# Optimization experiments

Measured on AMD Instinct MI355X. Metric: run time of the kernel, lower is better.

The kernel has to match this reference:

```python
import jax, jax.numpy as jnp
import numpy as np
from math import sqrt

V, D, H, HD, L, F, P, NL = 32000, 768, 12, 64, 12, 3072, 2048, 2
B, S = 8, 1024
EPS = 1e-5


def setup_inputs() -> dict:
    key = jax.random.key(0)
    ks = jax.random.split(key, 12)
    n = lambda k, sh: (jax.random.normal(k, sh, jnp.float32) * 0.02)
    return {
        'tokens': jax.random.randint(ks[0], (B, S), 0, V, dtype=jnp.int32),
        'tok_emb': n(ks[1], (V, D)),
        'pos_emb': n(ks[2], (P, D)),
        'emb_ln_s': jnp.ones((D,), jnp.float32), 'emb_ln_b': jnp.zeros((D,), jnp.float32),
        'Wq': n(ks[3], (L, H, D, HD)), 'bq': jnp.zeros((L, H, HD), jnp.float32),
        'Wk': n(ks[4], (L, H, D, HD)), 'bk': jnp.zeros((L, H, HD), jnp.float32),
        'Wv': n(ks[5], (L, H, D, HD)), 'bv': jnp.zeros((L, H, HD), jnp.float32),
        'Wo': n(ks[6], (L, D, D)), 'bo': jnp.zeros((L, D), jnp.float32),
        'ln1_s': jnp.ones((L, D), jnp.float32), 'ln1_b': jnp.zeros((L, D), jnp.float32),
        'ln2_s': jnp.ones((L, D), jnp.float32), 'ln2_b': jnp.zeros((L, D), jnp.float32),
        'W1': n(ks[7], (L, D, F)), 'b1': jnp.zeros((L, F), jnp.float32),
        'W2': n(ks[8], (L, F, D)), 'b2': jnp.zeros((L, D), jnp.float32),
        'Wc': n(ks[9], (D, NL)), 'bc': jnp.zeros((NL,), jnp.float32),
    }


def _ln(x, s, b):
    m = jnp.mean(x, -1, keepdims=True)
    v = jnp.mean((x - m) ** 2, -1, keepdims=True)
    return (x - m) * jax.lax.rsqrt(v + EPS) * s + b


def reference(tokens, tok_emb, pos_emb, emb_ln_s, emb_ln_b,
              Wq, bq, Wk, bk, Wv, bv, Wo, bo,
              ln1_s, ln1_b, ln2_s, ln2_b, W1, b1, W2, b2, Wc, bc):
    b, s = tokens.shape
    # embeddings (dropout is eval-mode identity)
    x = tok_emb[tokens] + pos_emb[:s][None, :, :]          # [b, s, D]
    x = _ln(x, emb_ln_s, emb_ln_b)
    scale = 1.0 / sqrt(HD)
    for l in range(L):
        xn = _ln(x, ln1_s[l], ln1_b[l])
        q = jnp.einsum('bsd,hdk->bhsk', xn, Wq[l]) + bq[l][:, None, :]
        k = jnp.einsum('bsd,hdk->bhsk', xn, Wk[l]) + bk[l][:, None, :]
        v = jnp.einsum('bsd,hdk->bhsk', xn, Wv[l]) + bv[l][:, None, :]
        scores = jnp.einsum('bhsk,bhtk->bhst', q, k) * scale   # [b,H,s,s]
        w = jax.nn.softmax(scores, axis=-1)
        o = jnp.einsum('bhst,bhtk->bhsk', w, v)                # [b,H,s,HD]
        o = o.transpose(0, 2, 1, 3).reshape(b, s, D)           # concat heads
        x = x + o @ Wo[l] + bo[l]
        xn = _ln(x, ln2_s[l], ln2_b[l])
        h = jax.nn.gelu(xn @ W1[l] + b1[l], approximate=False)
        x = x + h @ W2[l] + b2[l]
    # CLS token -> classifier (dropout identity)
    return x[:, 0, :] @ Wc + bc                                # [b, NL]
```

## Files before the change

### kernel.cpp

```cpp
#include <hip/hip_runtime.h>
#include <hip/hip_bf16.h>
#include <math.h>

#define B_   8
#define S_   1024
#define D_   768
#define H_   12
#define HD_  64
#define L_   12
#define F_   3072
#define NTOK 8192

typedef __bf16 bf16x8 __attribute__((ext_vector_type(8)));
typedef float  f32x4  __attribute__((ext_vector_type(4)));
typedef unsigned short u16;

static __device__ __forceinline__ unsigned short f2bf_bits(float f) {
    __hip_bfloat16 h = __float2bfloat16(f);
    return __builtin_bit_cast(unsigned short, h);
}
static __device__ __forceinline__ float bf2f(unsigned short u) {
    unsigned int t = ((unsigned int)u) << 16;
    return __builtin_bit_cast(float, t);
}
static __device__ __forceinline__ void gload16(const void* g, void* l) {
    __builtin_amdgcn_global_load_lds(
        (__attribute__((address_space(1))) void*)g,
        (__attribute__((address_space(3))) void*)l, 16, 0, 0);
}

__global__ __launch_bounds__(256)
void prep_layer_kernel(const float* __restrict__ Wq, const float* __restrict__ Wk,
                       const float* __restrict__ Wv, const float* __restrict__ Wo,
                       const float* __restrict__ W1, const float* __restrict__ W2,
                       int l, __hip_bfloat16* __restrict__ wbuf)
{
    const int id = blockIdx.x;
    const float* src; __hip_bfloat16* dst;
    int R, C, r0, c0;
    if (id < 432) {
        int dtile = id % 12, t = id / 12;
        int which = t / 12, h = t % 12;
        src = (which == 0 ? Wq : which == 1 ? Wk : Wv) + (size_t)(l*12 + h) * 768 * 64;
        dst = wbuf + (size_t)(which*768 + h*64) * 768;
        R = 768; C = 64; r0 = dtile * 64; c0 = 0;
    } else if (id < 576) {
        int t = id - 432;
        src = Wo + (size_t)l * 768 * 768;
        dst = wbuf + 1769472;
        R = 768; C = 768; r0 = (t / 12) * 64; c0 = (t % 12) * 64;
    } else if (id < 1152) {
        int t = id - 576;
        src = W1 + (size_t)l * 768 * 3072;
        dst = wbuf + 2359296;
        R = 768; C = 3072; r0 = (t % 12) * 64; c0 = (t / 12) * 64;
    } else {
        int t = id - 1152;
        src = W2 + (size_t)l * 3072 * 768;
        dst = wbuf + 4718592;
        R = 3072; C = 768; r0 = (t / 12) * 64; c0 = (t % 12) * 64;
    }
    __shared__ u16 T[64][68];
    const int t = threadIdx.x;
    const int row = t >> 2, part = t & 3;
#pragma unroll
    for (int j = 0; j < 4; ++j) {
        const int c4 = (part + j*4) * 4;
        float4 v = *(const float4*)(src + (size_t)(r0 + row) * C + c0 + c4);
        T[c4+0][row] = f2bf_bits(v.x);
        T[c4+1][row] = f2bf_bits(v.y);
        T[c4+2][row] = f2bf_bits(v.z);
        T[c4+3][row] = f2bf_bits(v.w);
    }
    __syncthreads();
    const int c = t >> 2;
    u16* drow = (u16*)dst + (size_t)(c0 + c) * R + r0;
#pragma unroll
    for (int j = 0; j < 4; ++j) {
        const int r4 = (part + j*4) * 4;
        ushort4 pk = *(const ushort4*)&T[c][r4];
        *(ushort4*)(drow + r4) = pk;
    }
}

__global__ __launch_bounds__(256)
void prep_bqkv_kernel(const float* __restrict__ bq, const float* __restrict__ bk,
                      const float* __restrict__ bv, float* __restrict__ bqkv)
{
    int i = blockIdx.x * 256 + threadIdx.x;
    int l = i / 2304, c = i % 2304;
    int which = c / 768, hk = c % 768;
    const float* src = which == 0 ? bq : which == 1 ? bk : bv;
    bqkv[i] = src[l*768 + hk];
}

__global__ __launch_bounds__(256)
void embed_ln_kernel(const int* __restrict__ tokens, const float* __restrict__ tok_emb,
                     const float* __restrict__ pos_emb, const float* __restrict__ gam,
                     const float* __restrict__ bet, float* __restrict__ x)
{
    const int row  = blockIdx.x*4 + (threadIdx.x >> 6);
    const int lane = threadIdx.x & 63;
    const int s    = row & (S_-1);
    const int tok  = tokens[row];
    const float* te = tok_emb + (size_t)tok * D_;
    const float* pe = pos_emb + (size_t)s   * D_;
    float v[12]; float s1 = 0.f, s2 = 0.f;
#pragma unroll
    for (int c = 0; c < 3; ++c) {
        const int base = c*256 + lane*4;
        float4 a = *(const float4*)(te + base);
        float4 p = *(const float4*)(pe + base);
        float t0 = a.x+p.x, t1 = a.y+p.y, t2 = a.z+p.z, t3 = a.w+p.w;
        v[c*4+0]=t0; v[c*4+1]=t1; v[c*4+2]=t2; v[c*4+3]=t3;
        s1 += t0+t1+t2+t3;
        s2 += t0*t0 + t1*t1 + t2*t2 + t3*t3;
    }
#pragma unroll
    for (int off = 32; off > 0; off >>= 1) { s1 += __shfl_xor(s1, off); s2 += __shfl_xor(s2, off); }
    const float mean = s1 * (1.f/768.f);
    const float rstd = rsqrtf(s2*(1.f/768.f) - mean*mean + 1e-5f);
    float* xr = x + (size_t)row * D_;
#pragma unroll
    for (int c = 0; c < 3; ++c) {
        const int base = c*256 + lane*4;
        float4 g = *(const float4*)(gam + base);
        float4 bb = *(const float4*)(bet + base);
        float4 o;
        o.x = (v[c*4+0]-mean)*rstd*g.x + bb.x;
        o.y = (v[c*4+1]-mean)*rstd*g.y + bb.y;
        o.z = (v[c*4+2]-mean)*rstd*g.z + bb.z;
        o.w = (v[c*4+3]-mean)*rstd*g.w + bb.w;
        *(float4*)(xr + base) = o;
    }
}

__global__ __launch_bounds__(256)
void ln_kernel(const float* __restrict__ xin, const float* __restrict__ gam,
               const float* __restrict__ bet, __hip_bfloat16* __restrict__ out)
{
    const int row  = blockIdx.x*4 + (threadIdx.x >> 6);
    const int lane = threadIdx.x & 63;
    const float* xr = xin + (size_t)row * D_;
    float v[12]; float s1 = 0.f, s2 = 0.f;
#pragma unroll
    for (int c = 0; c < 3; ++c) {
        float4 t = *(const float4*)(xr + c*256 + lane*4);
        v[c*4+0]=t.x; v[c*4+1]=t.y; v[c*4+2]=t.z; v[c*4+3]=t.w;
        s1 += t.x+t.y+t.z+t.w;
        s2 += t.x*t.x + t.y*t.y + t.z*t.z + t.w*t.w;
    }
#pragma unroll
    for (int off = 32; off > 0; off >>= 1) { s1 += __shfl_xor(s1, off); s2 += __shfl_xor(s2, off); }
    const float mean = s1 * (1.f/768.f);
    const float rstd = rsqrtf(s2*(1.f/768.f) - mean*mean + 1e-5f);
    unsigned short* op = (unsigned short*)out + (size_t)row * D_;
#pragma unroll
    for (int c = 0; c < 3; ++c) {
        const int base = c*256 + lane*4;
        float4 g = *(const float4*)(gam + base);
        float4 bb = *(const float4*)(bet + base);
        ushort4 pk;
        pk.x = f2bf_bits((v[c*4+0]-mean)*rstd*g.x + bb.x);
        pk.y = f2bf_bits((v[c*4+1]-mean)*rstd*g.y + bb.y);
        pk.z = f2bf_bits((v[c*4+2]-mean)*rstd*g.z + bb.z);
        pk.w = f2bf_bits((v[c*4+3]-mean)*rstd*g.w + bb.w);
        *(ushort4*)(op + base) = pk;
    }
}

template<int EPI>
__global__ __launch_bounds__(256)
void gemm_kernel(const __hip_bfloat16* __restrict__ A,
                 const __hip_bfloat16* __restrict__ Bt,
                 const float* __restrict__ bias,
                 __hip_bfloat16* __restrict__ outb,
                 __hip_bfloat16* __restrict__ outv,
                 int N, int K, int nTiles)
{
    __shared__ __align__(16) char smem[32768];
    __hip_bfloat16* As = (__hip_bfloat16*)smem;
    __hip_bfloat16* Bs = (__hip_bfloat16*)(smem + 16384);

    const int tid  = threadIdx.x;
    const int lane = tid & 63;
    const int wid  = tid >> 6;

    const int nwg   = gridDim.x;
    const int chunk = nwg >> 3;
    const int bid   = blockIdx.x;
    const int swz   = (bid & 7) * chunk + (bid >> 3);
    const int m0 = (swz / nTiles) * 128;
    const int n0 = (swz % nTiles) * 128;

    const int srow = wid*32 + (lane >> 3);
    const int scol = ((lane & 7) ^ (srow & 7)) * 8;
    const __hip_bfloat16* aSrc = A  + (size_t)(m0 + srow) * K + scol;
    const __hip_bfloat16* bSrc = Bt + (size_t)(n0 + srow) * K + scol;
    char* aDst = (char*)As + wid*4096 + lane*16;
    char* bDst = (char*)Bs + wid*4096 + lane*16;

    f32x4 acc[4][4] = {};
    const int wm = wid >> 1, wn = wid & 1;
    const int cl = lane & 15, hi = lane >> 4;

    for (int kt = 0; kt < K; kt += 64) {
        __syncthreads();
#pragma unroll
        for (int i = 0; i < 4; ++i)
            gload16(aSrc + kt + (size_t)i*8*K, aDst + i*1024);
#pragma unroll
        for (int i = 0; i < 4; ++i)
            gload16(bSrc + kt + (size_t)i*8*K, bDst + i*1024);
        __syncthreads();

#pragma unroll
        for (int kk = 0; kk < 2; ++kk) {
            bf16x8 af[4], bfr[4];
#pragma unroll
            for (int m = 0; m < 4; ++m) {
                int row  = wm*64 + m*16 + cl;
                int slot = ((kk<<2) + hi) ^ (row & 7);
                af[m] = *(const bf16x8*)((const char*)As + row*128 + slot*16);
            }
#pragma unroll
            for (int n = 0; n < 4; ++n) {
                int row  = wn*64 + n*16 + cl;
                int slot = ((kk<<2) + hi) ^ (row & 7);
                bfr[n] = *(const bf16x8*)((const char*)Bs + row*128 + slot*16);
            }
#pragma unroll
            for (int m = 0; m < 4; ++m)
#pragma unroll
                for (int n = 0; n < 4; ++n)
                    acc[m][n] = __builtin_amdgcn_mfma_f32_16x16x32_bf16(af[m], bfr[n], acc[m][n], 0, 0, 0);
        }
    }

    const bool vpath = (EPI == 0) && (n0 >= 1536);

    if (!vpath) {
        __syncthreads();
#pragma unroll
        for (int n = 0; n < 4; ++n) {
            const int col2 = wn*64 + n*16 + cl;
            const float bv = bias[n0 + col2];
#pragma unroll
            for (int m = 0; m < 4; ++m) {
#pragma unroll
                for (int i = 0; i < 4; ++i) {
                    const int row = wm*64 + m*16 + hi*4 + i;
                    float v = acc[m][n][i] + bv;
                    if constexpr (EPI == 1) {
                        const float y = 0.7978845608f * (v + 0.044715f*v*v*v);
                        const float e = __expf(-2.0f * fabsf(y));
                        const float th = (1.0f - e) / (1.0f + e);
                        v = 0.5f * v * (1.0f + copysignf(th, y));
                    }
                    *(u16*)(smem + row*256 + ((((col2 >> 3) ^ (row & 15))) << 4)
                                 + ((col2 & 7) << 1)) = f2bf_bits(v);
                }
            }
        }
        __syncthreads();
        const int strideN = (EPI == 0) ? 1536 : N;
        const int r  = tid >> 1;
        const int cb = tid & 1;
        char* dst = (char*)outb + ((size_t)(m0 + r) * strideN + n0) * 2;
#pragma unroll
        for (int j = 0; j < 8; ++j) {
            const int ch = cb + j*2;
            float4 vv = *(const float4*)(smem + r*256 + ((ch ^ (r & 15)) << 4));
            *(float4*)(dst + ch*16) = vv;
        }
    } else {
        __syncthreads();
#pragma unroll
        for (int n = 0; n < 4; ++n) {
            const int col = n0 + wn*64 + n*16 + cl;
            const float bv = bias[col];
            const int hdl = wn*64 + n*16 + cl;
#pragma unroll
            for (int m = 0; m < 4; ++m) {
                const int sl = wm*64 + m*16 + hi*4;
                ushort4 pk;
                pk.x = f2bf_bits(acc[m][n][0] + bv);
                pk.y = f2bf_bits(acc[m][n][1] + bv);
                pk.z = f2bf_bits(acc[m][n][2] + bv);
                pk.w = f2bf_bits(acc[m][n][3] + bv);
                *(ushort4*)(smem + hdl*256 + ((((sl >> 3) ^ (hdl & 15))) << 4) + (sl & 7)*2) = pk;
            }
        }
        __syncthreads();
        const int hdl2 = tid >> 1;
        const int sh   = (tid & 1) * 64;
        const int hdg  = (n0 - 1536) + hdl2;
        const int bb   = m0 >> 10;
        u16* dst = (u16*)outv + ((size_t)(bb*768) + hdg)*1024 + (m0 & 1023) + sh;
#pragma unroll
        for (int j = 0; j < 8; ++j) {
            const int slot = ((sh >> 3) + j) ^ (hdl2 & 15);
            *(float4*)((char*)dst + j*16) = *(const float4*)(smem + hdl2*256 + (slot << 4));
        }
    }
}

__global__ __launch_bounds__(256)
void gemm64_res_kernel(const __hip_bfloat16* __restrict__ A,
                       const __hip_bfloat16* __restrict__ Bt,
                       const float* __restrict__ bias,
                       float* __restrict__ outf,
                       int N, int K, int nTiles)
{
    __shared__ __align__(16) char smem[32768];
    __hip_bfloat16* As = (__hip_bfloat16*)smem;
    __hip_bfloat16* Bs = (__hip_bfloat16*)(smem + 8192);

    const int tid  = threadIdx.x;
    const int lane = tid & 63;
    const int wid  = tid >> 6;

    const int nwg   = gridDim.x;
    const int chunk = nwg >> 3;
    const int bid   = blockIdx.x;
    const int swz   = (bid & 7) * chunk + (bid >> 3);
    const int m0 = (swz / nTiles) * 64;
    const int n0 = (swz % nTiles) * 128;

    const int lrow = lane >> 3;
    const int scol = ((lane & 7) ^ lrow) * 8;
    const __hip_bfloat16* aSrc = A  + (size_t)(m0 + wid*16 + lrow) * K + scol;
    const __hip_bfloat16* bSrc = Bt + (size_t)(n0 + wid*32 + lrow) * K + scol;
    char* aDst = (char*)As + wid*2048 + lane*16;
    char* bDst = (char*)Bs + wid*4096 + lane*16;

    f32x4 acc[2][4] = {};
    const int wm = wid >> 1, wn = wid & 1;
    const int cl = lane & 15, hi = lane >> 4;

    for (int kt = 0; kt < K; kt += 64) {
        __syncthreads();
#pragma unroll
        for (int i = 0; i < 2; ++i)
            gload16(aSrc + kt + (size_t)i*8*K, aDst + i*1024);
#pragma unroll
        for (int i = 0; i < 4; ++i)
            gload16(bSrc + kt + (size_t)i*8*K, bDst + i*1024);
        __syncthreads();

#pragma unroll
        for (int kk = 0; kk < 2; ++kk) {
            bf16x8 af[2], bfr[4];
#pragma unroll
            for (int m = 0; m < 2; ++m) {
                int row  = wm*32 + m*16 + cl;
                int slot = ((kk<<2) + hi) ^ (row & 7);
                af[m] = *(const bf16x8*)((const char*)As + row*128 + slot*16);
            }
#pragma unroll
            for (int n = 0; n < 4; ++n) {
                int row  = wn*64 + n*16 + cl;
                int slot = ((kk<<2) + hi) ^ (row & 7);
                bfr[n] = *(const bf16x8*)((const char*)Bs + row*128 + slot*16);
            }
#pragma unroll
            for (int m = 0; m < 2; ++m)
#pragma unroll
                for (int n = 0; n < 4; ++n)
                    acc[m][n] = __builtin_amdgcn_mfma_f32_16x16x32_bf16(af[m], bfr[n], acc[m][n], 0, 0, 0);
        }
    }

    __syncthreads();
#pragma unroll
    for (int n = 0; n < 4; ++n) {
        const int col = wn*64 + n*16 + cl;
        const float bv = bias[n0 + col];
#pragma unroll
        for (int m = 0; m < 2; ++m) {
#pragma unroll
            for (int i = 0; i < 4; ++i) {
                const int row = wm*32 + m*16 + hi*4 + i;
                *(float*)(smem + row*512 + ((((col >> 2) ^ (row & 31))) << 4)
                               + ((col & 3) << 2)) = acc[m][n][i] + bv;
            }
        }
    }
    __syncthreads();
    const int r = tid >> 2;
    const int part = tid & 3;
    float* drow = outf + (size_t)(m0 + r) * N + n0;
#pragma unroll
    for (int j = 0; j < 8; ++j) {
        const int ch = part + j*4;
        f32x4 vv = *(const f32x4*)(smem + r*512 + ((ch ^ (r & 31)) << 4));
        float* dp = drow + ch*4;
        f32x4 g = *(const f32x4*)dp;
        g += vv;
        *(f32x4*)dp = g;
    }
}

__global__ __launch_bounds__(512)
void attn_kernel(const __hip_bfloat16* __restrict__ qkb, const __hip_bfloat16* __restrict__ vtb,
                 __hip_bfloat16* __restrict__ attno)
{
    __shared__ __align__(16) char Ks[2][8192];
    __shared__ __align__(16) char Vs[2][8192];
    __shared__ __align__(16) char Ps[16384];

    const u16* qk = (const u16*)qkb;
    const u16* vt = (const u16*)vtb;
    const int nwg = gridDim.x, bid = blockIdx.x, chunk = nwg >> 3;
    const int swz = (bid & 7) * chunk + (bid >> 3);
    const int bh = swz >> 3, qb = swz & 7;
    const int b = bh / H_, h = bh % H_;
    const int tid = threadIdx.x;
    const int lane = tid & 63, wid = tid >> 6;
    const int cl = lane & 15, hi = lane >> 4;
    const size_t browq = (size_t)(b*S_ + qb*128);

    bf16x8 qf[2];
    {
        const u16* qp = qk + (browq + wid*16 + cl)*1536 + h*64;
        qf[0] = *(const bf16x8*)(qp + hi*8);
        qf[1] = *(const bf16x8*)(qp + 32 + hi*8);
    }

    const int lrow = lane >> 3;
    const int scol = ((lane & 7) ^ lrow) * 8;
    const u16* kbase = qk + ((size_t)b*S_ + wid*8 + lrow)*1536 + 768 + h*64 + scol;
    const u16* vbase = vt + (((size_t)(b*H_ + h))*64 + wid*8 + lrow)*1024 + scol;
    const int ldst = wid*1024 + lane*16;

    f32x4 acc_o[4] = {};
    float m_run = -1e30f;
    float l_part[4] = {0.f, 0.f, 0.f, 0.f};
    char* pbase = Ps + wid*2048;

    {
        gload16(kbase, Ks[0] + ldst);
        gload16(vbase, Vs[0] + ldst);
    }

    for (int t = 0; t < 16; ++t) {
        __syncthreads();
        if (t < 15) {
            const int nb = (t+1) & 1;
            gload16(kbase + (size_t)(t+1)*64*1536, Ks[nb] + ldst);
            gload16(vbase + (t+1)*64,              Vs[nb] + ldst);
        }
        const char* ks = Ks[t & 1];
        const char* vs = Vs[t & 1];

        f32x4 sc[4] = {};
#pragma unroll
        for (int kk = 0; kk < 2; ++kk) {
            bf16x8 kf[4];
#pragma unroll
            for (int n = 0; n < 4; ++n) {
                const int row = n*16 + cl;
                kf[n] = *(const bf16x8*)(ks + row*128 + (((kk*4 + hi) ^ (cl & 7)) << 4));
            }
#pragma unroll
            for (int n = 0; n < 4; ++n)
                sc[n] = __builtin_amdgcn_mfma_f32_16x16x32_bf16(qf[kk], kf[n], sc[n], 0, 0, 0);
        }

#pragma unroll
        for (int n = 0; n < 4; ++n)
#pragma unroll
            for (int i = 0; i < 4; ++i)
                sc[n][i] *= 0.125f;

        float gmax = sc[0][0];
#pragma unroll
        for (int n = 0; n < 4; ++n)
#pragma unroll
            for (int i = 0; i < 4; ++i)
                gmax = fmaxf(gmax, sc[n][i]);
        gmax = fmaxf(gmax, __shfl_xor(gmax, 1));
        gmax = fmaxf(gmax, __shfl_xor(gmax, 2));
        gmax = fmaxf(gmax, __shfl_xor(gmax, 4));
        gmax = fmaxf(gmax, __shfl_xor(gmax, 8));
        if (gmax > m_run + 4.0f) {
            const float corr = __expf(m_run - gmax);
            m_run = gmax;
#pragma unroll
            for (int i = 0; i < 4; ++i) l_part[i] *= corr;
#pragma unroll
            for (int nd = 0; nd < 4; ++nd)
#pragma unroll
                for (int i = 0; i < 4; ++i)
                    acc_o[nd][i] *= corr;
        }

#pragma unroll
        for (int n = 0; n < 4; ++n) {
#pragma unroll
            for (int i = 0; i < 4; ++i) {
                const float e = __expf(sc[n][i] - m_run);
                l_part[i] += e;
                const int q = hi*4 + i;
                const int slot = (n*2 + (cl >> 3)) ^ (q & 7);
                *(u16*)(pbase + q*128 + slot*16 + (cl & 7)*2) = f2bf_bits(e);
            }
        }

        asm volatile("s_waitcnt lgkmcnt(0)" ::: "memory");
        __builtin_amdgcn_sched_barrier(0);

#pragma unroll
        for (int kk = 0; kk < 2; ++kk) {
            const bf16x8 pf = *(const bf16x8*)(pbase + cl*128 + (((kk*4 + hi) ^ (cl & 7)) << 4));
            bf16x8 vf[4];
#pragma unroll
            for (int nd = 0; nd < 4; ++nd) {
                const int d = nd*16 + cl;
                vf[nd] = *(const bf16x8*)(vs + d*128 + (((kk*4 + hi) ^ (d & 7)) << 4));
            }
#pragma unroll
            for (int nd = 0; nd < 4; ++nd)
                acc_o[nd] = __builtin_amdgcn_mfma_f32_16x16x32_bf16(pf, vf[nd], acc_o[nd], 0, 0, 0);
        }
    }

    u16* op = (u16*)attno;
#pragma unroll
    for (int i = 0; i < 4; ++i) {
        float l = l_part[i];
        l += __shfl_xor(l, 1);
        l += __shfl_xor(l, 2);
        l += __shfl_xor(l, 4);
        l += __shfl_xor(l, 8);
        const float inv = 1.f / l;
        const size_t row = browq + wid*16 + hi*4 + i;
#pragma unroll
        for (int nd = 0; nd < 4; ++nd)
            op[row*768 + h*64 + nd*16 + cl] = f2bf_bits(acc_o[nd][i] * inv);
    }
}

__global__ __launch_bounds__(256)
void cls_kernel(const float* __restrict__ x, const float* __restrict__ Wc,
                const float* __restrict__ bc, float* __restrict__ out)
{
    const int b = blockIdx.x;
    const float* xr = x + (size_t)b * S_ * D_;
    float a0 = 0.f, a1 = 0.f;
    for (int d = threadIdx.x; d < 768; d += 256) {
        float xv = xr[d];
        a0 += xv * Wc[d*2+0];
        a1 += xv * Wc[d*2+1];
    }
#pragma unroll
    for (int off = 32; off > 0; off >>= 1) { a0 += __shfl_xor(a0, off); a1 += __shfl_xor(a1, off); }
    __shared__ float r0[4], r1[4];
    const int w = threadIdx.x >> 6;
    if ((threadIdx.x & 63) == 0) { r0[w] = a0; r1[w] = a1; }
    __syncthreads();
    if (threadIdx.x == 0) {
        out[b*2+0] = r0[0]+r0[1]+r0[2]+r0[3] + bc[0];
        out[b*2+1] = r1[0]+r1[1]+r1[2]+r1[3] + bc[1];
    }
}

extern "C" void kernel_launch(void* const* d_in, const int* in_sizes, int n_in,
                              void* d_out, int out_size, void* d_ws, size_t ws_size,
                              hipStream_t stream)
{
    const int*   tokens  = (const int*)  d_in[0];
    const float* tok_emb = (const float*)d_in[1];
    const float* pos_emb = (const float*)d_in[2];
    const float* e_s     = (const float*)d_in[3];
    const float* e_b     = (const float*)d_in[4];
    const float* Wq      = (const float*)d_in[5];
    const float* bq      = (const float*)d_in[6];
    const float* Wk      = (const float*)d_in[7];
    const float* bk      = (const float*)d_in[8];
    const float* Wv      = (const float*)d_in[9];
    const float* bv      = (const float*)d_in[10];
    const float* Wo      = (const float*)d_in[11];
    const float* bo      = (const float*)d_in[12];
    const float* l1s     = (const float*)d_in[13];
    const float* l1b     = (const float*)d_in[14];
    const float* l2s     = (const float*)d_in[15];
    const float* l2b     = (const float*)d_in[16];
    const float* W1      = (const float*)d_in[17];
    const float* b1      = (const float*)d_in[18];
    const float* W2      = (const float*)d_in[19];
    const float* b2      = (const float*)d_in[20];
    const float* Wc      = (const float*)d_in[21];
    const float* bc      = (const float*)d_in[22];
    (void)in_sizes; (void)n_in; (void)out_size;

    if (ws_size < 102346752) return;

    char* ws = (char*)d_ws;
    __hip_bfloat16* wbuf = (__hip_bfloat16*)(ws + 0);
    float*          bqkv = (float*)(ws + 14155776);
    float*          x    = (float*)(ws + 14266368);
    __hip_bfloat16* xn   = (__hip_bfloat16*)(ws + 39432192);
    __hip_bfloat16* qk   = (__hip_bfloat16*)(ws + 52015104);
    __hip_bfloat16* vT   = (__hip_bfloat16*)(ws + 77180928);
    __hip_bfloat16* att  = (__hip_bfloat16*)(ws + 89763840);
    __hip_bfloat16* hbuf = qk;

    __hip_bfloat16* wqkv_t = wbuf;
    __hip_bfloat16* wo_t   = wbuf + 1769472;
    __hip_bfloat16* w1_t   = wbuf + 2359296;
    __hip_bfloat16* w2_t   = wbuf + 4718592;

    prep_bqkv_kernel<<<108, 256, 0, stream>>>(bq, bk, bv, bqkv);
    embed_ln_kernel<<<2048, 256, 0, stream>>>(tokens, tok_emb, pos_emb, e_s, e_b, x);

    for (int l = 0; l < L_; ++l) {
        prep_layer_kernel<<<1728, 256, 0, stream>>>(Wq, Wk, Wv, Wo, W1, W2, l, wbuf);
        ln_kernel<<<2048, 256, 0, stream>>>(x, l1s + l*768, l1b + l*768, xn);
        gemm_kernel<0><<<1152, 256, 0, stream>>>(xn, wqkv_t, bqkv + l*2304, qk, vT, 2304, 768, 18);
        attn_kernel<<<768, 512, 0, stream>>>(qk, vT, att);
        gemm64_res_kernel<<<768, 256, 0, stream>>>(att, wo_t, bo + l*768, x, 768, 768, 6);
        ln_kernel<<<2048, 256, 0, stream>>>(x, l2s + l*768, l2b + l*768, xn);
        gemm_kernel<1><<<1536, 256, 0, stream>>>(xn, w1_t, b1 + l*3072, hbuf, nullptr, 3072, 768, 24);
        gemm64_res_kernel<<<768, 256, 0, stream>>>(hbuf, w2_t, b2 + l*768, x, 768, 3072, 6);
    }
    cls_kernel<<<8, 256, 0, stream>>>(x, Wc, bc, (float*)d_out);
}
```

Before: 3.232 ms.

## Double-buffer GEMM shared tiles and unify on 64x128 tiles across all projections

```diff
diff --git a/kernel.cpp b/kernel.cpp
--- a/kernel.cpp
+++ b/kernel.cpp
@@ -176,11 +176,14 @@
                  const float* __restrict__ bias,
                  __hip_bfloat16* __restrict__ outb,
                  __hip_bfloat16* __restrict__ outv,
+                 float* __restrict__ outf,
                  int N, int K, int nTiles)
 {
-    __shared__ __align__(16) char smem[32768];
-    __hip_bfloat16* As = (__hip_bfloat16*)smem;
-    __hip_bfloat16* Bs = (__hip_bfloat16*)(smem + 16384);
+    __shared__ __align__(16) char smem[49152];
+    char* const As0 = smem;
+    char* const As1 = smem + 8192;
+    char* const Bs0 = smem + 16384;
+    char* const Bs1 = smem + 32768;
 
     const int tid  = threadIdx.x;
     const int lane = tid & 63;
@@ -190,66 +193,108 @@
     const int chunk = nwg >> 3;
     const int bid   = blockIdx.x;
     const int swz   = (bid & 7) * chunk + (bid >> 3);
-    const int m0 = (swz / nTiles) * 128;
+    const int m0 = (swz / nTiles) * 64;
     const int n0 = (swz % nTiles) * 128;
 
-    const int srow = wid*32 + (lane >> 3);
-    const int scol = ((lane & 7) ^ (srow & 7)) * 8;
-    const __hip_bfloat16* aSrc = A  + (size_t)(m0 + srow) * K + scol;
-    const __hip_bfloat16* bSrc = Bt + (size_t)(n0 + srow) * K + scol;
-    char* aDst = (char*)As + wid*4096 + lane*16;
-    char* bDst = (char*)Bs + wid*4096 + lane*16;
-
-    f32x4 acc[4][4] = {};
+    const int lrow = lane >> 3;
+    const int scol = ((lane & 7) ^ lrow) * 8;
+    const __hip_bfloat16* aSrc = A  + (size_t)(m0 + wid*16 + lrow) * K + scol;
+    const __hip_bfloat16* bSrc = Bt + (size_t)(n0 + wid*32 + lrow) * K + scol;
+    const int aOff = wid*2048 + lane*16;
+    const int bOff = wid*4096 + lane*16;
+
+    f32x4 acc[2][4] = {};
     const int wm = wid >> 1, wn = wid & 1;
     const int cl = lane & 15, hi = lane >> 4;
 
-    for (int kt = 0; kt < K; kt += 64) {
+#pragma unroll
+    for (int i = 0; i < 2; ++i)
+        gload16(aSrc + (size_t)i*8*K, As0 + aOff + i*1024);
+#pragma unroll
+    for (int i = 0; i < 4; ++i)
+        gload16(bSrc + (size_t)i*8*K, Bs0 + bOff + i*1024);
+
+    int buf = 0;
+    for (int kt = 0; kt < K; kt += 64, buf ^= 1) {
         __syncthreads();
-#pragma unroll
-        for (int i = 0; i < 4; ++i)
-            gload16(aSrc + kt + (size_t)i*8*K, aDst + i*1024);
-#pragma unroll
-        for (int i = 0; i < 4; ++i)
-            gload16(bSrc + kt + (size_t)i*8*K, bDst + i*1024);
-        __syncthreads();
+        if (kt + 64 < K) {
+            char* an = buf ? As0 : As1;
+            char* bn = buf ? Bs0 : Bs1;
+#pragma unroll
+            for (int i = 0; i < 2; ++i)
+                gload16(aSrc + kt + 64 + (size_t)i*8*K, an + aOff + i*1024);
+#pragma unroll
+            for (int i = 0; i < 4; ++i)
+                gload16(bSrc + kt + 64 + (size_t)i*8*K, bn + bOff + i*1024);
+        }
+        const char* ac = buf ? As1 : As0;
+        const char* bc = buf ? Bs1 : Bs0;
 
 #pragma unroll
         for (int kk = 0; kk < 2; ++kk) {
-            bf16x8 af[4], bfr[4];
-#pragma unroll
-            for (int m = 0; m < 4; ++m) {
-                int row  = wm*64 + m*16 + cl;
+            bf16x8 af[2], bfr[4];
+#pragma unroll
+            for (int m = 0; m < 2; ++m) {
+                int row  = wm*32 + m*16 + cl;
                 int slot = ((kk<<2) + hi) ^ (row & 7);
-                af[m] = *(const bf16x8*)((const char*)As + row*128 + slot*16);
+                af[m] = *(const bf16x8*)(ac + row*128 + slot*16);
             }
 #pragma unroll
             for (int n = 0; n < 4; ++n) {
                 int row  = wn*64 + n*16 + cl;
                 int slot = ((kk<<2) + hi) ^ (row & 7);
-                bfr[n] = *(const bf16x8*)((const char*)Bs + row*128 + slot*16);
-            }
-#pragma unroll
-            for (int m = 0; m < 4; ++m)
+                bfr[n] = *(const bf16x8*)(bc + row*128 + slot*16);
+            }
+#pragma unroll
+            for (int m = 0; m < 2; ++m)
 #pragma unroll
                 for (int n = 0; n < 4; ++n)
                     acc[m][n] = __builtin_amdgcn_mfma_f32_16x16x32_bf16(af[m], bfr[n], acc[m][n], 0, 0, 0);
         }
     }
 
+    __syncthreads();
+
     const bool vpath = (EPI == 0) && (n0 >= 1536);
 
-    if (!vpath) {
+    if constexpr (EPI == 2) {
+#pragma unroll
+        for (int n = 0; n < 4; ++n) {
+            const int col = wn*64 + n*16 + cl;
+            const float bv = bias[n0 + col];
+#pragma unroll
+            for (int m = 0; m < 2; ++m) {
+#pragma unroll
+                for (int i = 0; i < 4; ++i) {
+                    const int row = wm*32 + m*16 + hi*4 + i;
+                    *(float*)(smem + row*512 + ((((col >> 2) ^ (row & 31))) << 4)
+                                   + ((col & 3) << 2)) = acc[m][n][i] + bv;
+                }
+            }
+        }
         __syncthreads();
+        const int r = tid >> 2;
+        const int part = tid & 3;
+        float* drow = outf + (size_t)(m0 + r) * N + n0;
+#pragma unroll
+        for (int j = 0; j < 8; ++j) {
+            const int ch = part + j*4;
+            f32x4 vv = *(const f32x4*)(smem + r*512 + ((ch ^ (r & 31)) << 4));
+            float* dp = drow + ch*4;
+            f32x4 g = *(const f32x4*)dp;
+            g += vv;
+            *(f32x4*)dp = g;
+        }
+    } else if (!vpath) {
 #pragma unroll
         for (int n = 0; n < 4; ++n) {
             const int col2 = wn*64 + n*16 + cl;
             const float bv = bias[n0 + col2];
 #pragma unroll
-            for (int m = 0; m < 4; ++m) {
+            for (int m = 0; m < 2; ++m) {
 #pragma unroll
                 for (int i = 0; i < 4; ++i) {
-                    const int row = wm*64 + m*16 + hi*4 + i;
+                    const int row = wm*32 + m*16 + hi*4 + i;
                     float v = acc[m][n][i] + bv;
                     if constexpr (EPI == 1) {
                         const float y = 0.7978845608f * (v + 0.044715f*v*v*v);
@@ -264,140 +309,42 @@
         }
         __syncthreads();
         const int strideN = (EPI == 0) ? 1536 : N;
-        const int r  = tid >> 1;
-        const int cb = tid & 1;
-        char* dst = (char*)outb + ((size_t)(m0 + r) * strideN + n0) * 2;
-#pragma unroll
-        for (int j = 0; j < 8; ++j) {
-            const int ch = cb + j*2;
+        const int r  = tid >> 2;
+        const int part = tid & 3;
+        u16* dst = (u16*)outb + (size_t)(m0 + r) * strideN + n0;
+#pragma unroll
+        for (int j = 0; j < 4; ++j) {
+            const int ch = part + j*4;
             float4 vv = *(const float4*)(smem + r*256 + ((ch ^ (r & 15)) << 4));
-            *(float4*)(dst + ch*16) = vv;
+            *(float4*)((char*)dst + ch*16) = vv;
         }
     } else {
-        __syncthreads();
 #pragma unroll
         for (int n = 0; n < 4; ++n) {
-            const int col = n0 + wn*64 + n*16 + cl;
-            const float bv = bias[col];
             const int hdl = wn*64 + n*16 + cl;
-#pragma unroll
-            for (int m = 0; m < 4; ++m) {
-                const int sl = wm*64 + m*16 + hi*4;
+            const float bv = bias[n0 + hdl];
+#pragma unroll
+            for (int m = 0; m < 2; ++m) {
+                const int sl = wm*32 + m*16 + hi*4;
                 ushort4 pk;
                 pk.x = f2bf_bits(acc[m][n][0] + bv);
                 pk.y = f2bf_bits(acc[m][n][1] + bv);
                 pk.z = f2bf_bits(acc[m][n][2] + bv);
                 pk.w = f2bf_bits(acc[m][n][3] + bv);
-                *(ushort4*)(smem + hdl*256 + ((((sl >> 3) ^ (hdl & 15))) << 4) + (sl & 7)*2) = pk;
+                *(ushort4*)(smem + hdl*128 + ((((sl >> 3) ^ (hdl & 7))) << 4) + (sl & 7)*2) = pk;
             }
         }
         __syncthreads();
         const int hdl2 = tid >> 1;
-        const int sh   = (tid & 1) * 64;
+        const int sh   = (tid & 1) * 32;
         const int hdg  = (n0 - 1536) + hdl2;
         const int bb   = m0 >> 10;
         u16* dst = (u16*)outv + ((size_t)(bb*768) + hdg)*1024 + (m0 & 1023) + sh;
 #pragma unroll
-        for (int j = 0; j < 8; ++j) {
-            const int slot = ((sh >> 3) + j) ^ (hdl2 & 15);
-            *(float4*)((char*)dst + j*16) = *(const float4*)(smem + hdl2*256 + (slot << 4));
-        }
-    }
-}
-
-__global__ __launch_bounds__(256)
-void gemm64_res_kernel(const __hip_bfloat16* __restrict__ A,
-                       const __hip_bfloat16* __restrict__ Bt,
-                       const float* __restrict__ bias,
-                       float* __restrict__ outf,
-                       int N, int K, int nTiles)
-{
-    __shared__ __align__(16) char smem[32768];
-    __hip_bfloat16* As = (__hip_bfloat16*)smem;
-    __hip_bfloat16* Bs = (__hip_bfloat16*)(smem + 8192);
-
-    const int tid  = threadIdx.x;
-    const int lane = tid & 63;
-    const int wid  = tid >> 6;
-
-    const int nwg   = gridDim.x;
-    const int chunk = nwg >> 3;
-    const int bid   = blockIdx.x;
-    const int swz   = (bid & 7) * chunk + (bid >> 3);
-    const int m0 = (swz / nTiles) * 64;
-    const int n0 = (swz % nTiles) * 128;
-
-    const int lrow = lane >> 3;
-    const int scol = ((lane & 7) ^ lrow) * 8;
-    const __hip_bfloat16* aSrc = A  + (size_t)(m0 + wid*16 + lrow) * K + scol;
-    const __hip_bfloat16* bSrc = Bt + (size_t)(n0 + wid*32 + lrow) * K + scol;
-    char* aDst = (char*)As + wid*2048 + lane*16;
-    char* bDst = (char*)Bs + wid*4096 + lane*16;
-
-    f32x4 acc[2][4] = {};
-    const int wm = wid >> 1, wn = wid & 1;
-    const int cl = lane & 15, hi = lane >> 4;
-
-    for (int kt = 0; kt < K; kt += 64) {
-        __syncthreads();
-#pragma unroll
-        for (int i = 0; i < 2; ++i)
-            gload16(aSrc + kt + (size_t)i*8*K, aDst + i*1024);
-#pragma unroll
-        for (int i = 0; i < 4; ++i)
-            gload16(bSrc + kt + (size_t)i*8*K, bDst + i*1024);
-        __syncthreads();
-
-#pragma unroll
-        for (int kk = 0; kk < 2; ++kk) {
-            bf16x8 af[2], bfr[4];
-#pragma unroll
-            for (int m = 0; m < 2; ++m) {
-                int row  = wm*32 + m*16 + cl;
-                int slot = ((kk<<2) + hi) ^ (row & 7);
-                af[m] = *(const bf16x8*)((const char*)As + row*128 + slot*16);
-            }
-#pragma unroll
-            for (int n = 0; n < 4; ++n) {
-                int row  = wn*64 + n*16 + cl;
-                int slot = ((kk<<2) + hi) ^ (row & 7);
-                bfr[n] = *(const bf16x8*)((const char*)Bs + row*128 + slot*16);
-            }
-#pragma unroll
-            for (int m = 0; m < 2; ++m)
-#pragma unroll
-                for (int n = 0; n < 4; ++n)
-                    acc[m][n] = __builtin_amdgcn_mfma_f32_16x16x32_bf16(af[m], bfr[n], acc[m][n], 0, 0, 0);
-        }
-    }
-
-    __syncthreads();
-#pragma unroll
-    for (int n = 0; n < 4; ++n) {
-        const int col = wn*64 + n*16 + cl;
-        const float bv = bias[n0 + col];
-#pragma unroll
-        for (int m = 0; m < 2; ++m) {
-#pragma unroll
-            for (int i = 0; i < 4; ++i) {
-                const int row = wm*32 + m*16 + hi*4 + i;
-                *(float*)(smem + row*512 + ((((col >> 2) ^ (row & 31))) << 4)
-                               + ((col & 3) << 2)) = acc[m][n][i] + bv;
-            }
-        }
-    }
-    __syncthreads();
-    const int r = tid >> 2;
-    const int part = tid & 3;
-    float* drow = outf + (size_t)(m0 + r) * N + n0;
-#pragma unroll
-    for (int j = 0; j < 8; ++j) {
-        const int ch = part + j*4;
-        f32x4 vv = *(const f32x4*)(smem + r*512 + ((ch ^ (r & 31)) << 4));
-        float* dp = drow + ch*4;
-        f32x4 g = *(const f32x4*)dp;
-        g += vv;
-        *(f32x4*)dp = g;
+        for (int j = 0; j < 4; ++j) {
+            const int slot = ((sh >> 3) + j) ^ (hdl2 & 7);
+            *(float4*)((char*)dst + j*16) = *(const float4*)(smem + hdl2*128 + (slot << 4));
+        }
     }
 }
 
@@ -617,12 +564,12 @@
     for (int l = 0; l < L_; ++l) {
         prep_layer_kernel<<<1728, 256, 0, stream>>>(Wq, Wk, Wv, Wo, W1, W2, l, wbuf);
         ln_kernel<<<2048, 256, 0, stream>>>(x, l1s + l*768, l1b + l*768, xn);
-        gemm_kernel<0><<<1152, 256, 0, stream>>>(xn, wqkv_t, bqkv + l*2304, qk, vT, 2304, 768, 18);
+        gemm_kernel<0><<<2304, 256, 0, stream>>>(xn, wqkv_t, bqkv + l*2304, qk, vT, nullptr, 2304, 768, 18);
         attn_kernel<<<768, 512, 0, stream>>>(qk, vT, att);
-        gemm64_res_kernel<<<768, 256, 0, stream>>>(att, wo_t, bo + l*768, x, 768, 768, 6);
+        gemm_kernel<2><<<768, 256, 0, stream>>>(att, wo_t, bo + l*768, nullptr, nullptr, x, 768, 768, 6);
         ln_kernel<<<2048, 256, 0, stream>>>(x, l2s + l*768, l2b + l*768, xn);
-        gemm_kernel<1><<<1536, 256, 0, stream>>>(xn, w1_t, b1 + l*3072, hbuf, nullptr, 3072, 768, 24);
-        gemm64_res_kernel<<<768, 256, 0, stream>>>(hbuf, w2_t, b2 + l*768, x, 768, 3072, 6);
+        gemm_kernel<1><<<3072, 256, 0, stream>>>(xn, w1_t, b1 + l*3072, hbuf, nullptr, nullptr, 3072, 768, 24);
+        gemm_kernel<2><<<768, 256, 0, stream>>>(hbuf, w2_t, b2 + l*768, nullptr, nullptr, x, 768, 3072, 6);
     }
     cls_kernel<<<8, 256, 0, stream>>>(x, Wc, bc, (float*)d_out);
 }
```

Result: faster. 3.005 ms (-7.0%).

## Double-buffer LDS tiles in GEMM kernels to overlap global loads with MFMA

Applied to the files above, without the earlier changes.

```diff
diff --git a/kernel.cpp b/kernel.cpp
--- a/kernel.cpp
+++ b/kernel.cpp
@@ -171,16 +171,18 @@
 
 template<int EPI>
 __global__ __launch_bounds__(256)
-void gemm_kernel(const __hip_bfloat16* __restrict__ A,
-                 const __hip_bfloat16* __restrict__ Bt,
-                 const float* __restrict__ bias,
-                 __hip_bfloat16* __restrict__ outb,
-                 __hip_bfloat16* __restrict__ outv,
-                 int N, int K, int nTiles)
+void gemm128_kernel(const __hip_bfloat16* __restrict__ A,
+                    const __hip_bfloat16* __restrict__ Bt,
+                    const float* __restrict__ bias,
+                    __hip_bfloat16* __restrict__ outb,
+                    __hip_bfloat16* __restrict__ outv,
+                    int N, int K, int nTiles)
 {
     __shared__ __align__(16) char smem[32768];
-    __hip_bfloat16* As = (__hip_bfloat16*)smem;
-    __hip_bfloat16* Bs = (__hip_bfloat16*)(smem + 16384);
+    char* const As0 = smem;
+    char* const As1 = smem + 8192;
+    char* const Bs0 = smem + 16384;
+    char* const Bs1 = smem + 24576;
 
     const int tid  = threadIdx.x;
     const int lane = tid & 63;
@@ -193,54 +195,66 @@
     const int m0 = (swz / nTiles) * 128;
     const int n0 = (swz % nTiles) * 128;
 
-    const int srow = wid*32 + (lane >> 3);
-    const int scol = ((lane & 7) ^ (srow & 7)) * 8;
-    const __hip_bfloat16* aSrc = A  + (size_t)(m0 + srow) * K + scol;
-    const __hip_bfloat16* bSrc = Bt + (size_t)(n0 + srow) * K + scol;
-    char* aDst = (char*)As + wid*4096 + lane*16;
-    char* bDst = (char*)Bs + wid*4096 + lane*16;
+    const int l4 = lane >> 2;
+    const int sswz = ((lane & 3) ^ ((l4 >> 1) & 3)) * 8;
+    const __hip_bfloat16* aSrc = A  + (size_t)(m0 + wid*32 + l4) * K + sswz;
+    const __hip_bfloat16* bSrc = Bt + (size_t)(n0 + wid*32 + l4) * K + sswz;
+    const int sOff = wid*2048 + lane*16;
 
     f32x4 acc[4][4] = {};
     const int wm = wid >> 1, wn = wid & 1;
     const int cl = lane & 15, hi = lane >> 4;
 
-    for (int kt = 0; kt < K; kt += 64) {
+    int aoff[4], boff[4];
+#pragma unroll
+    for (int m = 0; m < 4; ++m) {
+        const int row = wm*64 + m*16 + cl;
+        aoff[m] = row*64 + ((hi ^ ((row >> 1) & 3)) << 4);
+    }
+#pragma unroll
+    for (int n = 0; n < 4; ++n) {
+        const int row = wn*64 + n*16 + cl;
+        boff[n] = row*64 + ((hi ^ ((row >> 1) & 3)) << 4);
+    }
+
+#pragma unroll
+    for (int i = 0; i < 2; ++i) {
+        gload16(aSrc + (size_t)i*16*K, As0 + sOff + i*1024);
+        gload16(bSrc + (size_t)i*16*K, Bs0 + sOff + i*1024);
+    }
+
+    int buf = 0;
+    for (int kt = 0; kt < K; kt += 32, buf ^= 1) {
         __syncthreads();
-#pragma unroll
-        for (int i = 0; i < 4; ++i)
-            gload16(aSrc + kt + (size_t)i*8*K, aDst + i*1024);
-#pragma unroll
-        for (int i = 0; i < 4; ++i)
-            gload16(bSrc + kt + (size_t)i*8*K, bDst + i*1024);
-        __syncthreads();
-
-#pragma unroll
-        for (int kk = 0; kk < 2; ++kk) {
-            bf16x8 af[4], bfr[4];
-#pragma unroll
-            for (int m = 0; m < 4; ++m) {
-                int row  = wm*64 + m*16 + cl;
-                int slot = ((kk<<2) + hi) ^ (row & 7);
-                af[m] = *(const bf16x8*)((const char*)As + row*128 + slot*16);
-            }
-#pragma unroll
-            for (int n = 0; n < 4; ++n) {
-                int row  = wn*64 + n*16 + cl;
-                int slot = ((kk<<2) + hi) ^ (row & 7);
-                bfr[n] = *(const bf16x8*)((const char*)Bs + row*128 + slot*16);
-            }
-#pragma unroll
-            for (int m = 0; m < 4; ++m)
-#pragma unroll
-                for (int n = 0; n < 4; ++n)
-                    acc[m][n] = __builtin_amdgcn_mfma_f32_16x16x32_bf16(af[m], bfr[n], acc[m][n], 0, 0, 0);
-        }
-    }
+        if (kt + 32 < K) {
+            char* an = buf ? As0 : As1;
+            char* bn = buf ? Bs0 : Bs1;
+#pragma unroll
+            for (int i = 0; i < 2; ++i) {
+                gload16(aSrc + kt + 32 + (size_t)i*16*K, an + sOff + i*1024);
+                gload16(bSrc + kt + 32 + (size_t)i*16*K, bn + sOff + i*1024);
+            }
+        }
+        const char* ac = buf ? As1 : As0;
+        const char* bc = buf ? Bs1 : Bs0;
+
+        bf16x8 af[4], bfr[4];
+#pragma unroll
+        for (int m = 0; m < 4; ++m) af[m]  = *(const bf16x8*)(ac + aoff[m]);
+#pragma unroll
+        for (int n = 0; n < 4; ++n) bfr[n] = *(const bf16x8*)(bc + boff[n]);
+#pragma unroll
+        for (int m = 0; m < 4; ++m)
+#pragma unroll
+            for (int n = 0; n < 4; ++n)
+                acc[m][n] = __builtin_amdgcn_mfma_f32_16x16x32_bf16(af[m], bfr[n], acc[m][n], 0, 0, 0);
+    }
+
+    __syncthreads();
 
     const bool vpath = (EPI == 0) && (n0 >= 1536);
 
     if (!vpath) {
-        __syncthreads();
 #pragma unroll
         for (int n = 0; n < 4; ++n) {
             const int col2 = wn*64 + n*16 + cl;
@@ -274,12 +288,10 @@
             *(float4*)(dst + ch*16) = vv;
         }
     } else {
-        __syncthreads();
 #pragma unroll
         for (int n = 0; n < 4; ++n) {
-            const int col = n0 + wn*64 + n*16 + cl;
-            const float bv = bias[col];
             const int hdl = wn*64 + n*16 + cl;
+            const float bv = bias[n0 + hdl];
 #pragma unroll
             for (int m = 0; m < 4; ++m) {
                 const int sl = wm*64 + m*16 + hi*4;
@@ -306,15 +318,17 @@
 }
 
 __global__ __launch_bounds__(256)
-void gemm64_res_kernel(const __hip_bfloat16* __restrict__ A,
-                       const __hip_bfloat16* __restrict__ Bt,
-                       const float* __restrict__ bias,
-                       float* __restrict__ outf,
-                       int N, int K, int nTiles)
-{
-    __shared__ __align__(16) char smem[32768];
-    __hip_bfloat16* As = (__hip_bfloat16*)smem;
-    __hip_bfloat16* Bs = (__hip_bfloat16*)(smem + 8192);
+void gemm_res_kernel(const __hip_bfloat16* __restrict__ A,
+                     const __hip_bfloat16* __restrict__ Bt,
+                     const float* __restrict__ bias,
+                     float* __restrict__ outf,
+                     int N, int K, int nTiles)
+{
+    __shared__ __align__(16) char smem[49152];
+    char* const As0 = smem;
+    char* const As1 = smem + 8192;
+    char* const Bs0 = smem + 16384;
+    char* const Bs1 = smem + 32768;
 
     const int tid  = threadIdx.x;
     const int lane = tid & 63;
@@ -331,22 +345,35 @@
     const int scol = ((lane & 7) ^ lrow) * 8;
     const __hip_bfloat16* aSrc = A  + (size_t)(m0 + wid*16 + lrow) * K + scol;
     const __hip_bfloat16* bSrc = Bt + (size_t)(n0 + wid*32 + lrow) * K + scol;
-    char* aDst = (char*)As + wid*2048 + lane*16;
-    char* bDst = (char*)Bs + wid*4096 + lane*16;
+    const int aOff = wid*2048 + lane*16;
+    const int bOff = wid*4096 + lane*16;
 
     f32x4 acc[2][4] = {};
     const int wm = wid >> 1, wn = wid & 1;
     const int cl = lane & 15, hi = lane >> 4;
 
-    for (int kt = 0; kt < K; kt += 64) {
+#pragma unroll
+    for (int i = 0; i < 2; ++i)
+        gload16(aSrc + (size_t)i*8*K, As0 + aOff + i*1024);
+#pragma unroll
+    for (int i = 0; i < 4; ++i)
+        gload16(bSrc + (size_t)i*8*K, Bs0 + bOff + i*1024);
+
+    int buf = 0;
+    for (int kt = 0; kt < K; kt += 64, buf ^= 1) {
         __syncthreads();
-#pragma unroll
-        for (int i = 0; i < 2; ++i)
-            gload16(aSrc + kt + (size_t)i*8*K, aDst + i*1024);
-#pragma unroll
-        for (int i = 0; i < 4; ++i)
-            gload16(bSrc + kt + (size_t)i*8*K, bDst + i*1024);
-        __syncthreads();
+        if (kt + 64 < K) {
+            char* an = buf ? As0 : As1;
+            char* bn = buf ? Bs0 : Bs1;
+#pragma unroll
+            for (int i = 0; i < 2; ++i)
+                gload16(aSrc + kt + 64 + (size_t)i*8*K, an + aOff + i*1024);
+#pragma unroll
+            for (int i = 0; i < 4; ++i)
+                gload16(bSrc + kt + 64 + (size_t)i*8*K, bn + bOff + i*1024);
+        }
+        const char* ac = buf ? As1 : As0;
+        const char* bc = buf ? Bs1 : Bs0;
 
 #pragma unroll
         for (int kk = 0; kk < 2; ++kk) {
@@ -355,13 +382,13 @@
             for (int m = 0; m < 2; ++m) {
                 int row  = wm*32 + m*16 + cl;
                 int slot = ((kk<<2) + hi) ^ (row & 7);
-                af[m] = *(const bf16x8*)((const char*)As + row*128 + slot*16);
+                af[m] = *(const bf16x8*)(ac + row*128 + slot*16);
             }
 #pragma unroll
             for (int n = 0; n < 4; ++n) {
                 int row  = wn*64 + n*16 + cl;
                 int slot = ((kk<<2) + hi) ^ (row & 7);
-                bfr[n] = *(const bf16x8*)((const char*)Bs + row*128 + slot*16);
+                bfr[n] = *(const bf16x8*)(bc + row*128 + slot*16);
             }
 #pragma unroll
             for (int m = 0; m < 2; ++m)
@@ -372,6 +399,7 @@
     }
 
     __syncthreads();
+
 #pragma unroll
     for (int n = 0; n < 4; ++n) {
         const int col = wn*64 + n*16 + cl;
@@ -617,12 +645,12 @@
     for (int l = 0; l < L_; ++l) {
         prep_layer_kernel<<<1728, 256, 0, stream>>>(Wq, Wk, Wv, Wo, W1, W2, l, wbuf);
         ln_kernel<<<2048, 256, 0, stream>>>(x, l1s + l*768, l1b + l*768, xn);
-        gemm_kernel<0><<<1152, 256, 0, stream>>>(xn, wqkv_t, bqkv + l*2304, qk, vT, 2304, 768, 18);
+        gemm128_kernel<0><<<1152, 256, 0, stream>>>(xn, wqkv_t, bqkv + l*2304, qk, vT, 2304, 768, 18);
         attn_kernel<<<768, 512, 0, stream>>>(qk, vT, att);
-        gemm64_res_kernel<<<768, 256, 0, stream>>>(att, wo_t, bo + l*768, x, 768, 768, 6);
+        gemm_res_kernel<<<768, 256, 0, stream>>>(att, wo_t, bo + l*768, x, 768, 768, 6);
         ln_kernel<<<2048, 256, 0, stream>>>(x, l2s + l*768, l2b + l*768, xn);
-        gemm_kernel<1><<<1536, 256, 0, stream>>>(xn, w1_t, b1 + l*3072, hbuf, nullptr, 3072, 768, 24);
-        gemm64_res_kernel<<<768, 256, 0, stream>>>(hbuf, w2_t, b2 + l*768, x, 768, 3072, 6);
+        gemm128_kernel<1><<<1536, 256, 0, stream>>>(xn, w1_t, b1 + l*3072, hbuf, nullptr, 3072, 768, 24);
+        gemm_res_kernel<<<768, 256, 0, stream>>>(hbuf, w2_t, b2 + l*768, x, 768, 3072, 6);
     }
     cls_kernel<<<8, 256, 0, stream>>>(x, Wc, bc, (float*)d_out);
 }
```

After: 3.065 ms. 1.05x faster.
